# Performance work log

Measured on AMD Instinct MI355X. Metric: run time of the kernel, lower is better.

The kernel has to match this reference:

```python
import jax, jax.numpy as jnp
import numpy as np

# VoxelGrid constants (create_empty not shown in source; fixed to a realistic dense grid)
W, L, H = 64, 64, 64
VOXEL_SIZE = 0.05
ORIGIN = 0.0  # per-axis origin, same for all batches
ROUNDING_OFFSET = 0.5
MIN_POINTS_PER_VOXEL = 10


def setup_inputs() -> dict:
    key = jax.random.key(0)
    k1, k2 = jax.random.split(key)
    B, C, N = 4, 32, 200_000
    extent = W * VOXEL_SIZE  # 3.2
    # uniform coords slightly extending past the grid so a few points are OOB
    point_coordinates = jax.random.uniform(
        k1, (B, 3, N), jnp.float32, minval=-0.02, maxval=extent + 0.02)
    point_attributes = jax.random.normal(k2, (B, C, N), jnp.float32)
    return {"point_coordinates": point_coordinates,
            "point_attributes": point_attributes}


def reference(point_coordinates, point_attributes):
    B, C, N = point_attributes.shape
    V = W * L * H
    bounds = jnp.array([W, L, H], jnp.int32)

    # point -> integer voxel coordinates (origin = 0)
    coords = jnp.floor((point_coordinates - ORIGIN) / VOXEL_SIZE
                       + ROUNDING_OFFSET).astype(jnp.int32)      # [B,3,N]
    in_bounds = jnp.all((coords >= 0) & (coords < bounds[None, :, None]),
                        axis=1)                                   # [B,N]
    flat = coords[:, 0] * (L * H) + coords[:, 1] * H + coords[:, 2]
    # route OOB points to segment V which is dropped by segment ops
    flat = jnp.where(in_bounds, flat, V)                          # [B,N]

    def per_batch(idx, attrs, mask):
        # idx [N] int32, attrs [C,N], mask [N] bool
        counts = jax.ops.segment_sum(mask.astype(jnp.int32), idx,
                                     num_segments=V)              # [V]
        vals = jnp.where(mask[None, :], attrs, -jnp.inf)          # [C,N]
        pooled = jax.ops.segment_max(vals.T, idx, num_segments=V).T  # [C,V]
        pooled = jnp.where(counts[None, :] > 0, pooled, jnp.zeros_like(pooled))
        occ = (counts >= MIN_POINTS_PER_VOXEL).astype(attrs.dtype)   # [V]
        return pooled, occ

    data, occ = jax.vmap(per_batch)(flat, point_attributes, in_bounds)
    voxeldata = data.reshape(B, C, W, L, H)
    voxeloccupancy = occ.reshape(B, 1, W, L, H)
    return voxeldata, voxeloccupancy
```

## Files before the change

### kernel.cpp

```cpp
#include <hip/hip_runtime.h>
#include <math.h>


#define GW 64
#define GL 64
#define GH 64
#define GV (GW * GL * GH)
#define NB 4
#define MIN_PTS 10

__device__ __forceinline__ int bin_coord(float x) {
    float m = __fmul_rn(x, 20.0f);
    float r = __fadd_rn(m, 0.5f);
    return (int)floorf(r);
}

__global__ void zero_kernel(uint4* __restrict__ p, int n4) {
    int i = blockIdx.x * blockDim.x + threadIdx.x;
    if (i < n4) p[i] = make_uint4(0u, 0u, 0u, 0u);
}

__global__ void hist_kernel(const float* __restrict__ coords,
                            int* __restrict__ counts,
                            int* __restrict__ vox,
                            int* __restrict__ rank,
                            int N) {
    int n = blockIdx.x * blockDim.x + threadIdx.x;
    int b = blockIdx.y;
    if (n >= N) return;
    const float* pc = coords + (size_t)b * 3 * N;
    int ix = bin_coord(pc[n]);
    int iy = bin_coord(pc[n + N]);
    int iz = bin_coord(pc[n + 2 * N]);
    bool ok = (unsigned)ix < (unsigned)GW && (unsigned)iy < (unsigned)GL &&
              (unsigned)iz < (unsigned)GH;
    int v = ok ? ((ix << 12) | (iy << 6) | iz) : -1;
    vox[(size_t)b * N + n] = v;
    if (ok) rank[(size_t)b * N + n] = atomicAdd(&counts[b * GV + v], 1);
}

__global__ void scan_blocks_kernel(const int* __restrict__ counts,
                                   int* __restrict__ offsets,
                                   int* __restrict__ blocksums) {
    __shared__ int lds[256];
    int t = threadIdx.x;
    int base = blockIdx.x * 1024 + t * 4;
    int4 c = *(const int4*)&counts[base];
    int s0 = c.x, s1 = s0 + c.y, s2 = s1 + c.z, s3 = s2 + c.w;
    lds[t] = s3;
    __syncthreads();
    for (int d = 1; d < 256; d <<= 1) {
        int v = (t >= d) ? lds[t - d] : 0;
        __syncthreads();
        if (t >= d) lds[t] += v;
        __syncthreads();
    }
    int excl = (t > 0) ? lds[t - 1] : 0;
    int4 o;
    o.x = excl; o.y = excl + s0; o.z = excl + s1; o.w = excl + s2;
    *(int4*)&offsets[base] = o;
    if (t == 255) blocksums[blockIdx.x] = lds[255];
}

__global__ void scan_sums_kernel(int* __restrict__ blocksums) {
    __shared__ int lds[256];
    int t = threadIdx.x;
    int4 c = *(const int4*)&blocksums[t * 4];
    int s0 = c.x, s1 = s0 + c.y, s2 = s1 + c.z, s3 = s2 + c.w;
    lds[t] = s3;
    __syncthreads();
    for (int d = 1; d < 256; d <<= 1) {
        int v = (t >= d) ? lds[t - d] : 0;
        __syncthreads();
        if (t >= d) lds[t] += v;
        __syncthreads();
    }
    int excl = (t > 0) ? lds[t - 1] : 0;
    int4 o;
    o.x = excl; o.y = excl + s0; o.z = excl + s1; o.w = excl + s2;
    *(int4*)&blocksums[t * 4] = o;
}

__global__ void scan_add_kernel(int* __restrict__ offsets,
                                const int* __restrict__ blocksums) {
    int i = blockIdx.x * blockDim.x + threadIdx.x;
    int s = blocksums[(i * 4) >> 10];
    int4 o = *(int4*)&offsets[i * 4];
    o.x += s; o.y += s; o.z += s; o.w += s;
    *(int4*)&offsets[i * 4] = o;
}

__global__ void sortscatter_kernel(const float* __restrict__ attrs,
                                   const int* __restrict__ vox,
                                   const int* __restrict__ rank,
                                   const int* __restrict__ offsets,
                                   float* __restrict__ sortedT,
                                   size_t sortedStride,
                                   int b0, int N) {
    int n = blockIdx.x * blockDim.x + threadIdx.x;
    int b = b0 + blockIdx.y;
    if (n >= N) return;
    int v = vox[(size_t)b * N + n];
    if (v < 0) return;
    int base = offsets[b * GV];
    int pos = offsets[b * GV + v] + rank[(size_t)b * N + n] - base;
    const float* pa = attrs + (size_t)b * 32 * N + n;
    float* dst = sortedT + (size_t)blockIdx.y * sortedStride + (size_t)pos * 32;
#pragma unroll
    for (int c = 0; c < 32; c += 4) {
        float4 w;
        w.x = pa[(size_t)(c + 0) * N];
        w.y = pa[(size_t)(c + 1) * N];
        w.z = pa[(size_t)(c + 2) * N];
        w.w = pa[(size_t)(c + 3) * N];
        *(float4*)&dst[c] = w;
    }
}

__global__ void segmaxT_kernel(const float* __restrict__ sortedT,
                               const int* __restrict__ counts,
                               const int* __restrict__ offsets,
                               float* __restrict__ vdata,
                               float* __restrict__ occ,
                               size_t sortedStride,
                               int b0) {
    int v = blockIdx.x * blockDim.x + threadIdx.x;
    int b = b0 + blockIdx.y;
    int bv = b * GV + v;
    int cnt = counts[bv];
    int off = offsets[bv] - offsets[b * GV];
    const float* src = sortedT + (size_t)blockIdx.y * sortedStride
                               + (size_t)off * 32;
    float4 m[8];
#pragma unroll
    for (int j = 0; j < 8; ++j)
        m[j] = make_float4(-INFINITY, -INFINITY, -INFINITY, -INFINITY);
    for (int k = 0; k < cnt; ++k) {
        const float4* p = (const float4*)(src + (size_t)k * 32);
#pragma unroll
        for (int j = 0; j < 8; ++j) {
            float4 x = p[j];
            m[j].x = fmaxf(m[j].x, x.x);
            m[j].y = fmaxf(m[j].y, x.y);
            m[j].z = fmaxf(m[j].z, x.z);
            m[j].w = fmaxf(m[j].w, x.w);
        }
    }
    float* out = vdata + (((size_t)b * 32) << 18) + v;
    bool nz = cnt > 0;
#pragma unroll
    for (int j = 0; j < 8; ++j) {
        out[((size_t)(4 * j + 0)) << 18] = nz ? m[j].x : 0.0f;
        out[((size_t)(4 * j + 1)) << 18] = nz ? m[j].y : 0.0f;
        out[((size_t)(4 * j + 2)) << 18] = nz ? m[j].z : 0.0f;
        out[((size_t)(4 * j + 3)) << 18] = nz ? m[j].w : 0.0f;
    }
    occ[bv] = (cnt >= MIN_PTS) ? 1.0f : 0.0f;
}


__global__ void scatter_idx_kernel(const int* __restrict__ vox,
                                   const int* __restrict__ rank,
                                   const int* __restrict__ offsets,
                                   int* __restrict__ sorted_idx,
                                   int N) {
    int n = blockIdx.x * blockDim.x + threadIdx.x;
    int b = blockIdx.y;
    if (n >= N) return;
    int v = vox[(size_t)b * N + n];
    if (v < 0) return;
    sorted_idx[offsets[b * GV + v] + rank[(size_t)b * N + n]] = n;
}

__global__ void segmax_kernel(const float* __restrict__ attrs,
                              const int* __restrict__ counts,
                              const int* __restrict__ offsets,
                              const int* __restrict__ sorted_idx,
                              float* __restrict__ vdata,
                              float* __restrict__ occ,
                              int N) {
    int t = blockIdx.x * blockDim.x + threadIdx.x;
    int v = t & (GV - 1);
    int c = (t >> 18) & 31;
    int b = t >> 23;
    int bv = (b << 18) | v;
    int cnt = counts[bv];
    int off = offsets[bv];
    const float* row = attrs + ((size_t)(b * 32 + c)) * N;
    float m = -INFINITY;
    for (int k = 0; k < cnt; ++k) {
        m = fmaxf(m, row[sorted_idx[off + k]]);
    }
    vdata[((size_t)(b * 32 + c) << 18) | v] = (cnt > 0) ? m : 0.0f;
    if (c == 0) occ[bv] = (cnt >= MIN_PTS) ? 1.0f : 0.0f;
}

__device__ __forceinline__ unsigned enc_f32(float f) {
    unsigned u = __float_as_uint(f);
    return (u & 0x80000000u) ? ~u : (u | 0x80000000u);
}
__device__ __forceinline__ float dec_f32(unsigned u) {
    return (u & 0x80000000u) ? __uint_as_float(u & 0x7FFFFFFFu)
                             : __uint_as_float(~u);
}

__global__ void init_kernel(uint4* __restrict__ data4, uint4* __restrict__ cnt4,
                            int nData4, int nCnt4) {
    int i = blockIdx.x * blockDim.x + threadIdx.x;
    uint4 z = make_uint4(0u, 0u, 0u, 0u);
    if (i < nData4) data4[i] = z;
    else if (i < nData4 + nCnt4) cnt4[i - nData4] = z;
}

__global__ void scatter_kernel(const float* __restrict__ coords,
                               const float* __restrict__ attrs,
                               unsigned* __restrict__ bits,
                               int* __restrict__ counts,
                               int N, int C) {
    int n = blockIdx.x * blockDim.x + threadIdx.x;
    int b = blockIdx.y;
    if (n >= N) return;
    const float* pc = coords + (size_t)b * 3 * N;
    int ix = bin_coord(pc[n]);
    int iy = bin_coord(pc[n + N]);
    int iz = bin_coord(pc[n + 2 * N]);
    if ((unsigned)ix >= (unsigned)GW || (unsigned)iy >= (unsigned)GL ||
        (unsigned)iz >= (unsigned)GH)
        return;
    int v = (ix << 12) | (iy << 6) | iz;
    atomicAdd(&counts[b * GV + v], 1);
    const float* pa = attrs + (size_t)b * C * N + n;
    unsigned* pb = bits + (size_t)b * C * GV + v;
    for (int c = 0; c < C; ++c)
        atomicMax(&pb[(size_t)c * GV], enc_f32(pa[(size_t)c * N]));
}

__global__ void finalize_kernel(unsigned* __restrict__ data,
                                const int* __restrict__ counts,
                                float* __restrict__ occ, int C) {
    int i = blockIdx.x * blockDim.x + threadIdx.x;
    int nData4 = NB * C * GV / 4;
    int nOcc4 = NB * GV / 4;
    if (i < nData4) {
        int idx = i << 2;
        int v = idx & (GV - 1);
        int b = idx / (C * GV);
        int4 cv = *(const int4*)&counts[b * GV + v];
        uint4 u = *(const uint4*)&data[idx];
        float4 r;
        r.x = cv.x > 0 ? dec_f32(u.x) : 0.0f;
        r.y = cv.y > 0 ? dec_f32(u.y) : 0.0f;
        r.z = cv.z > 0 ? dec_f32(u.z) : 0.0f;
        r.w = cv.w > 0 ? dec_f32(u.w) : 0.0f;
        *(float4*)&data[idx] = r;
    } else if (i < nData4 + nOcc4) {
        int j = (i - nData4) << 2;
        int4 cv = *(const int4*)&counts[j];
        float4 r;
        r.x = cv.x >= MIN_PTS ? 1.0f : 0.0f;
        r.y = cv.y >= MIN_PTS ? 1.0f : 0.0f;
        r.z = cv.z >= MIN_PTS ? 1.0f : 0.0f;
        r.w = cv.w >= MIN_PTS ? 1.0f : 0.0f;
        *(float4*)&occ[j] = r;
    }
}

extern "C" void kernel_launch(void* const* d_in, const int* in_sizes, int n_in,
                              void* d_out, int out_size, void* d_ws, size_t ws_size,
                              hipStream_t stream) {
    const float* coords = (const float*)d_in[0];
    const float* attrs  = (const float*)d_in[1];
    int N = in_sizes[0] / (NB * 3);
    int C = in_sizes[1] / (NB * N);

    size_t wsCommon = (size_t)(2 * NB * GV + 4096 + 2 * NB * N) * 4;
    size_t oneT  = (size_t)N * 32 * 4;
    size_t fullT = (size_t)NB * N * 32 * 4;
    size_t wsV1  = wsCommon + (size_t)NB * N * 4;

    if (C == 32 && ws_size >= wsCommon + oneT) {
        int* counts    = (int*)d_ws;
        int* offsets   = counts + (size_t)NB * GV;
        int* blocksums = offsets + (size_t)NB * GV;
        int* vox       = blocksums + 4096;
        int* rank      = vox + (size_t)NB * N;
        float* sortedT = (float*)(rank + (size_t)NB * N);
        float* vdata   = (float*)d_out;
        float* occ     = (float*)d_out + (size_t)NB * 32 * GV;

        int nCnt4 = NB * GV / 4;
        zero_kernel<<<(nCnt4 + 255) / 256, 256, 0, stream>>>((uint4*)counts,
                                                             nCnt4);
        dim3 pgrid((N + 255) / 256, NB);
        hist_kernel<<<pgrid, 256, 0, stream>>>(coords, counts, vox, rank, N);

        scan_blocks_kernel<<<NB * GV / 1024, 256, 0, stream>>>(counts, offsets,
                                                               blocksums);
        scan_sums_kernel<<<1, 256, 0, stream>>>(blocksums);
        scan_add_kernel<<<NB * GV / 1024, 256, 0, stream>>>(offsets, blocksums);

        if (ws_size >= wsCommon + fullT) {
            sortscatter_kernel<<<dim3((N + 255) / 256, NB), 256, 0, stream>>>(
                attrs, vox, rank, offsets, sortedT, (size_t)N * 32, 0, N);
            segmaxT_kernel<<<dim3(GV / 256, NB), 256, 0, stream>>>(
                sortedT, counts, offsets, vdata, occ, (size_t)N * 32, 0);
        } else {
            for (int b = 0; b < NB; ++b) {
                sortscatter_kernel<<<dim3((N + 255) / 256, 1), 256, 0, stream>>>(
                    attrs, vox, rank, offsets, sortedT, 0, b, N);
                segmaxT_kernel<<<dim3(GV / 256, 1), 256, 0, stream>>>(
                    sortedT, counts, offsets, vdata, occ, 0, b);
            }
        }
    } else if (C == 32 && ws_size >= wsV1) {
        int* counts     = (int*)d_ws;
        int* offsets    = counts + (size_t)NB * GV;
        int* blocksums  = offsets + (size_t)NB * GV;
        int* vox        = blocksums + 4096;
        int* rank       = vox + (size_t)NB * N;
        int* sorted_idx = rank + (size_t)NB * N;
        float* vdata    = (float*)d_out;
        float* occ      = (float*)d_out + (size_t)NB * 32 * GV;

        int nCnt4 = NB * GV / 4;
        zero_kernel<<<(nCnt4 + 255) / 256, 256, 0, stream>>>((uint4*)counts,
                                                             nCnt4);
        dim3 pgrid((N + 255) / 256, NB);
        hist_kernel<<<pgrid, 256, 0, stream>>>(coords, counts, vox, rank, N);

        scan_blocks_kernel<<<NB * GV / 1024, 256, 0, stream>>>(counts, offsets,
                                                               blocksums);
        scan_sums_kernel<<<1, 256, 0, stream>>>(blocksums);
        scan_add_kernel<<<NB * GV / 1024, 256, 0, stream>>>(offsets, blocksums);

        scatter_idx_kernel<<<pgrid, 256, 0, stream>>>(vox, rank, offsets,
                                                      sorted_idx, N);

        int segThreads = NB * 32 * GV;
        segmax_kernel<<<segThreads / 256, 256, 0, stream>>>(
            attrs, counts, offsets, sorted_idx, vdata, occ, N);
    } else {
        unsigned* bits = (unsigned*)d_out;
        float* occ = (float*)d_out + (size_t)NB * C * GV;
        int* counts = (int*)d_ws;
        int nData4 = NB * C * GV / 4;
        int nCnt4 = NB * GV / 4;
        int initTotal = nData4 + nCnt4;
        init_kernel<<<(initTotal + 255) / 256, 256, 0, stream>>>(
            (uint4*)d_out, (uint4*)d_ws, nData4, nCnt4);
        dim3 sgrid((N + 255) / 256, NB);
        scatter_kernel<<<sgrid, 256, 0, stream>>>(coords, attrs, bits, counts,
                                                  N, C);
        finalize_kernel<<<(initTotal + 255) / 256, 256, 0, stream>>>(
            bits, counts, occ, C);
    }
}
```

Baseline: 364.4 us.

## Stage scatter and segment-max through LDS for coalesced global accesses

```diff
diff --git a/kernel.cpp b/kernel.cpp
--- a/kernel.cpp
+++ b/kernel.cpp
@@ -90,74 +90,97 @@
     *(int4*)&offsets[i * 4] = o;
 }
 
-__global__ void sortscatter_kernel(const float* __restrict__ attrs,
-                                   const int* __restrict__ vox,
-                                   const int* __restrict__ rank,
-                                   const int* __restrict__ offsets,
-                                   float* __restrict__ sortedT,
-                                   size_t sortedStride,
-                                   int b0, int N) {
-    int n = blockIdx.x * blockDim.x + threadIdx.x;
+__global__ void sortscatter2_kernel(const float* __restrict__ attrs,
+                                    const int* __restrict__ vox,
+                                    const int* __restrict__ rank,
+                                    const int* __restrict__ offsets,
+                                    float* __restrict__ sortedT,
+                                    size_t sortedStride,
+                                    int b0, int N) {
+    __shared__ float lds[4][64 * 33];
+    __shared__ int posb[4][64];
+    int t = threadIdx.x;
+    int w = t >> 6;
+    int l = t & 63;
+    int n = blockIdx.x * 256 + t;
     int b = b0 + blockIdx.y;
-    if (n >= N) return;
-    int v = vox[(size_t)b * N + n];
-    if (v < 0) return;
-    int base = offsets[b * GV];
-    int pos = offsets[b * GV + v] + rank[(size_t)b * N + n] - base;
-    const float* pa = attrs + (size_t)b * 32 * N + n;
-    float* dst = sortedT + (size_t)blockIdx.y * sortedStride + (size_t)pos * 32;
+
+    int pos = -1;
+    if (n < N) {
+        int v = vox[(size_t)b * N + n];
+        if (v >= 0) {
+            int base = offsets[b * GV];
+            pos = offsets[b * GV + v] + rank[(size_t)b * N + n] - base;
+        }
+    }
+    posb[w][l] = pos;
+
+    if (n < N) {
+        const float* pa = attrs + (size_t)b * 32 * N + n;
+        float* row = &lds[w][l * 33];
 #pragma unroll
-    for (int c = 0; c < 32; c += 4) {
-        float4 w;
-        w.x = pa[(size_t)(c + 0) * N];
-        w.y = pa[(size_t)(c + 1) * N];
-        w.z = pa[(size_t)(c + 2) * N];
-        w.w = pa[(size_t)(c + 3) * N];
-        *(float4*)&dst[c] = w;
-    }
-}
-
-__global__ void segmaxT_kernel(const float* __restrict__ sortedT,
+        for (int c = 0; c < 32; ++c)
+            row[c] = pa[(size_t)c * N];
+    }
+    __syncthreads();
+
+    float* dbase = sortedT + (size_t)blockIdx.y * sortedStride;
+    int j = l & 7;
+#pragma unroll
+    for (int s = 0; s < 8; ++s) {
+        int q = s * 8 + (l >> 3);
+        int p = posb[w][q];
+        if (p >= 0) {
+            const float* src = &lds[w][q * 33 + j * 4];
+            float4 val = make_float4(src[0], src[1], src[2], src[3]);
+            *(float4*)&dbase[(size_t)p * 32 + j * 4] = val;
+        }
+    }
+}
+
+__global__ void segmax2_kernel(const float* __restrict__ sortedT,
                                const int* __restrict__ counts,
                                const int* __restrict__ offsets,
                                float* __restrict__ vdata,
                                float* __restrict__ occ,
                                size_t sortedStride,
                                int b0) {
-    int v = blockIdx.x * blockDim.x + threadIdx.x;
+    __shared__ float acc[64 * 33];
+    __shared__ int cntv[64];
+    int t = threadIdx.x;
+    int w = t >> 6;
+    int lane = t & 63;
+    int g = lane >> 5;
+    int c = lane & 31;
     int b = b0 + blockIdx.y;
-    int bv = b * GV + v;
-    int cnt = counts[bv];
-    int off = offsets[bv] - offsets[b * GV];
-    const float* src = sortedT + (size_t)blockIdx.y * sortedStride
-                               + (size_t)off * 32;
-    float4 m[8];
+    int v0 = blockIdx.x * 64;
+    int batchbase = offsets[b * GV];
+    const float* sbase = sortedT + (size_t)blockIdx.y * sortedStride;
+
 #pragma unroll
-    for (int j = 0; j < 8; ++j)
-        m[j] = make_float4(-INFINITY, -INFINITY, -INFINITY, -INFINITY);
-    for (int k = 0; k < cnt; ++k) {
-        const float4* p = (const float4*)(src + (size_t)k * 32);
+    for (int pp = 0; pp < 8; ++pp) {
+        int vl = w * 16 + pp * 2 + g;
+        int bv = b * GV + v0 + vl;
+        int cnt = counts[bv];
+        int off = offsets[bv] - batchbase;
+        const float* src = sbase + (size_t)off * 32 + c;
+        float m = -INFINITY;
+        for (int k = 0; k < cnt; ++k)
+            m = fmaxf(m, src[(size_t)k * 32]);
+        acc[vl * 33 + c] = (cnt > 0) ? m : 0.0f;
+        if (c == 0) cntv[vl] = cnt;
+    }
+    __syncthreads();
+
+    int vv = v0 + lane;
 #pragma unroll
-        for (int j = 0; j < 8; ++j) {
-            float4 x = p[j];
-            m[j].x = fmaxf(m[j].x, x.x);
-            m[j].y = fmaxf(m[j].y, x.y);
-            m[j].z = fmaxf(m[j].z, x.z);
-            m[j].w = fmaxf(m[j].w, x.w);
-        }
-    }
-    float* out = vdata + (((size_t)b * 32) << 18) + v;
-    bool nz = cnt > 0;
-#pragma unroll
-    for (int j = 0; j < 8; ++j) {
-        out[((size_t)(4 * j + 0)) << 18] = nz ? m[j].x : 0.0f;
-        out[((size_t)(4 * j + 1)) << 18] = nz ? m[j].y : 0.0f;
-        out[((size_t)(4 * j + 2)) << 18] = nz ? m[j].z : 0.0f;
-        out[((size_t)(4 * j + 3)) << 18] = nz ? m[j].w : 0.0f;
-    }
-    occ[bv] = (cnt >= MIN_PTS) ? 1.0f : 0.0f;
-}
-
+    for (int cc = 0; cc < 8; ++cc) {
+        int ch = cc * 4 + w;
+        vdata[(((size_t)(b * 32 + ch)) << 18) + vv] = acc[lane * 33 + ch];
+    }
+    if (t < 64)
+        occ[b * GV + v0 + t] = (cntv[t] >= MIN_PTS) ? 1.0f : 0.0f;
+}
 
 __global__ void scatter_idx_kernel(const int* __restrict__ vox,
                                    const int* __restrict__ rank,
@@ -300,15 +323,15 @@
         scan_add_kernel<<<NB * GV / 1024, 256, 0, stream>>>(offsets, blocksums);
 
         if (ws_size >= wsCommon + fullT) {
-            sortscatter_kernel<<<dim3((N + 255) / 256, NB), 256, 0, stream>>>(
+            sortscatter2_kernel<<<dim3((N + 255) / 256, NB), 256, 0, stream>>>(
                 attrs, vox, rank, offsets, sortedT, (size_t)N * 32, 0, N);
-            segmaxT_kernel<<<dim3(GV / 256, NB), 256, 0, stream>>>(
+            segmax2_kernel<<<dim3(GV / 64, NB), 256, 0, stream>>>(
                 sortedT, counts, offsets, vdata, occ, (size_t)N * 32, 0);
         } else {
             for (int b = 0; b < NB; ++b) {
-                sortscatter_kernel<<<dim3((N + 255) / 256, 1), 256, 0, stream>>>(
+                sortscatter2_kernel<<<dim3((N + 255) / 256, 1), 256, 0, stream>>>(
                     attrs, vox, rank, offsets, sortedT, 0, b, N);
-                segmaxT_kernel<<<dim3(GV / 256, 1), 256, 0, stream>>>(
+                segmax2_kernel<<<dim3(GV / 64, 1), 256, 0, stream>>>(
                     sortedT, counts, offsets, vdata, occ, 0, b);
             }
         }
```

Measured after the change: 335.7 us. 1.09x faster.
